# Optimization experiments

Hardware: AMD Instinct MI355X
Metric: run time of the kernel (lower is better)

## Reference

```python
import jax, jax.numpy as jnp
import numpy as np

N_NODES = 50000
N_EDGES = 800000
FEAT = 64
HID = 128
N_TYPES = 4
N_REL = 3
N_LAYERS = 2
LN_EPS = 1e-5


def setup_inputs() -> dict:
    key = jax.random.key(0)
    ks = jax.random.split(key, 20)
    inp = {
        "z": jax.random.randint(ks[0], (N_NODES,), 0, 100, dtype=jnp.int32),
        "node_type": jax.random.randint(ks[1], (N_NODES,), 0, N_TYPES, dtype=jnp.int32),
        "edge_index": jax.random.randint(ks[2], (2, N_EDGES), 0, N_NODES, dtype=jnp.int32),
        "edge_type": jax.random.randint(ks[3], (N_EDGES,), 0, N_REL, dtype=jnp.int32),
        # learned parameters
        "z_embed": jax.random.normal(ks[4], (100, FEAT), jnp.float32),
        "enc_w1": jax.random.normal(ks[5], (N_TYPES, FEAT, HID), jnp.float32) * 0.05,
        "enc_b1": jnp.zeros((N_TYPES, HID), jnp.float32),
        "enc_w2": jax.random.normal(ks[6], (N_TYPES, HID, HID), jnp.float32) * 0.05,
        "enc_b2": jnp.zeros((N_TYPES, HID), jnp.float32),
        "lin_w": jax.random.normal(ks[7], (N_LAYERS, HID, HID), jnp.float32) * 0.05,
        "lin_b": jnp.zeros((N_LAYERS, HID), jnp.float32),
        "rel_w": jax.random.normal(ks[8], (N_LAYERS, N_REL, HID, HID), jnp.float32) * 0.05,
        "ln_g": jnp.ones((N_LAYERS, HID), jnp.float32),
        "ln_b": jnp.zeros((N_LAYERS, HID), jnp.float32),
        "reg_w": jax.random.normal(ks[9], (HID, 1), jnp.float32) * 0.05,
        "reg_b": jnp.zeros((1,), jnp.float32),
    }
    return inp


def _layer_norm(x, g, b):
    mu = jnp.mean(x, axis=-1, keepdims=True)
    var = jnp.mean((x - mu) ** 2, axis=-1, keepdims=True)
    return (x - mu) * jax.lax.rsqrt(var + LN_EPS) * g + b


def reference(z, node_type, edge_index, edge_type, z_embed, enc_w1, enc_b1,
              enc_w2, enc_b2, lin_w, lin_b, rel_w, ln_g, ln_b, reg_w, reg_b):
    n = z.shape[0]
    # FeatureBuilder (site_ads=None path): atomic-number embedding lookup
    raw = z_embed[z]  # [N, FEAT]
    # TypeSpecificEncoder: run all 4 type MLPs, select per node by node_type
    h = jax.nn.relu(jnp.einsum('nd,tdh->nth', raw, enc_w1) + enc_b1)  # [N,T,H]
    enc_all = jnp.einsum('nth,tho->nto', h, enc_w2) + enc_b2           # [N,T,H]
    x = jnp.take_along_axis(enc_all, node_type[:, None, None].astype(jnp.int32), axis=1)[:, 0, :]

    src, dst = edge_index[0], edge_index[1]
    deg = jax.ops.segment_sum(jnp.ones((edge_type.shape[0],), x.dtype), dst, num_segments=n)
    deg = jnp.clip(deg, 1.0, None)[:, None]  # [N,1]

    for l in range(N_LAYERS):
        out = jnp.zeros_like(x)
        x_src = x[src]  # [E, H] gathered source features
        for r in range(N_REL):
            mask = (edge_type == r).astype(x.dtype)[:, None]
            msg = (x_src * mask) @ rel_w[l, r]  # [E, H]
            out = out + jax.ops.segment_sum(msg, dst, num_segments=n)
        out = out / deg
        x = _layer_norm(x @ lin_w[l] + lin_b[l] + out, ln_g[l], ln_b[l])

    pooled = jnp.mean(x, axis=0)  # mean pooling, mask = all ones
    return pooled @ reg_w + reg_b  # [1]
```

## Files before the change

kernel.cpp:

```cpp
#include <hip/hip_runtime.h>

#define N_NODES 50000
#define N_EDGES 800000
#define FEAT 64
#define HID 128
#define N_TYPES 4
#define N_REL 3
#define N_LAYERS 2
#define LN_EPS 1e-5f
#define NROWS 50016
#define NG32 1563
#define CAP 64
#define NBKT 196
#define CAP1 4608
#define EPB 4096
#define BINCAP 56
#define WT_STRIDE 136

typedef __attribute__((ext_vector_type(8))) short bf16x8;
typedef __attribute__((ext_vector_type(16))) float f32x16;

static __device__ inline unsigned short f2bf(float f) {
    unsigned int u = __float_as_uint(f);
    return (unsigned short)((u + 0x7fffu + ((u >> 16) & 1u)) >> 16);
}
static __device__ inline unsigned int packbf2(float lo, float hi) {
    return (unsigned int)f2bf(lo) | ((unsigned int)f2bf(hi) << 16);
}

__global__ __launch_bounds__(256) void bin1_kernel(const int* __restrict__ src,
                                                   const int* __restrict__ dst,
                                                   const int* __restrict__ et,
                                                   int* __restrict__ bcnt,
                                                   int* __restrict__ bucket) {
    __shared__ int lbin[NBKT * BINCAP];
    __shared__ int lcnt[NBKT];
    __shared__ int lbase[NBKT];
    for (int i = threadIdx.x; i < NBKT; i += 256) lcnt[i] = 0;
    __syncthreads();
    int base = blockIdx.x * EPB;
#pragma unroll
    for (int i = 0; i < EPB / 256; ++i) {
        int e = base + i * 256 + threadIdx.x;
        if (e < N_EDGES) {
            int d = dst[e];
            int b = d >> 8;
            int v = src[e] | (et[e] << 16) | ((d & 255) << 18);
            int pos = atomicAdd(&lcnt[b], 1);
            if (pos < BINCAP) lbin[b * BINCAP + pos] = v;
        }
    }
    __syncthreads();
    if (threadIdx.x < NBKT) {
        int c = min(lcnt[threadIdx.x], BINCAP);
        lcnt[threadIdx.x] = c;
        lbase[threadIdx.x] = atomicAdd(&bcnt[threadIdx.x], c);
    }
    __syncthreads();
    int wv = threadIdx.x >> 6, ln = threadIdx.x & 63;
    for (int b = wv; b < NBKT; b += 4) {
        int c = lcnt[b];
        if (ln < c) {
            int gp = lbase[b] + ln;
            if (gp < CAP1) bucket[b * CAP1 + gp] = lbin[b * BINCAP + ln];
        }
    }
}

__global__ __launch_bounds__(256) void build2_kernel(const int* __restrict__ bcnt,
                                                     const int* __restrict__ bucket,
                                                     int* __restrict__ cnt,
                                                     int* __restrict__ payload) {
    __shared__ int lcnt[256];
    lcnt[threadIdx.x] = 0;
    __syncthreads();
    int b = blockIdx.x;
    int n0 = b << 8;
    int cb = min(bcnt[b], CAP1);
    const int* bk = bucket + b * CAP1;
    for (int i = threadIdx.x; i < cb; i += 256) {
        int v = bk[i];
        int dl = (v >> 18) & 255;
        int pos = atomicAdd(&lcnt[dl], 1);
        if (pos < CAP) payload[((n0 + dl) << 6) + pos] = v & 0x3FFFF;
    }
    __syncthreads();
    int node = n0 + threadIdx.x;
    if (node < N_NODES) cnt[node] = min(lcnt[threadIdx.x], CAP);
}

__global__ __launch_bounds__(256) void prep_weights_kernel(const float* __restrict__ rel_w,
                                                           const float* __restrict__ lin_w,
                                                           unsigned short* __restrict__ wbuf) {
    int idx = blockIdx.x * 256 + threadIdx.x;
    if (idx >= 2 * 4 * HID * HID) return;
    int k = idx & 127;
    int col = (idx >> 7) & 127;
    int lm = idx >> 14;
    int l = lm >> 2, mat = lm & 3;
    float w = (mat < 3) ? rel_w[(((size_t)l * 3 + mat) * HID + k) * HID + col]
                        : lin_w[((size_t)l * HID + k) * HID + col];
    wbuf[(size_t)lm * HID * WT_STRIDE + col * WT_STRIDE + k] = f2bf(w);
}

__global__ __launch_bounds__(128) void enc_table_kernel(const float* __restrict__ z_embed,
                                                        const float* __restrict__ w1,
                                                        const float* __restrict__ b1,
                                                        const float* __restrict__ w2,
                                                        const float* __restrict__ b2,
                                                        unsigned short* __restrict__ xt) {
    int zi = blockIdx.x >> 2;
    int t = blockIdx.x & 3;
    int j = threadIdx.x;
    __shared__ float h[HID];
    float acc = b1[t * HID + j];
#pragma unroll 8
    for (int k = 0; k < FEAT; ++k)
        acc = fmaf(z_embed[zi * FEAT + k], w1[((size_t)t * FEAT + k) * HID + j], acc);
    h[j] = fmaxf(acc, 0.0f);
    __syncthreads();
    float acc2 = b2[t * HID + j];
#pragma unroll 8
    for (int k = 0; k < HID; ++k)
        acc2 = fmaf(h[k], w2[(size_t)t * HID * HID + k * HID + j], acc2);
    xt[blockIdx.x * HID + j] = f2bf(acc2);
}

__global__ __launch_bounds__(256) void node_fill_kernel(const int* __restrict__ z,
                                                        const int* __restrict__ nt,
                                                        const unsigned int* __restrict__ xtu,
                                                        unsigned int* __restrict__ xbu) {
    int idx = blockIdx.x * blockDim.x + threadIdx.x;
    int node = idx >> 6;
    if (node >= N_NODES) return;
    int lane = idx & 63;
    int combo = z[node] * 4 + nt[node];
    xbu[node * 64 + lane] = xtu[combo * 64 + lane];
}

__global__ __launch_bounds__(256) void gather3_kernel(const int* __restrict__ cnt,
                                                      const int* __restrict__ payload,
                                                      const uint4* __restrict__ xb4,
                                                      uint4* __restrict__ s0,
                                                      uint4* __restrict__ s1,
                                                      uint4* __restrict__ s2) {
    int tid = blockIdx.x * 256 + threadIdx.x;
    int node = tid >> 4;
    int l16 = tid & 15;
    int cn = min(cnt[node], CAP);
    float inv = 1.0f / (float)max(cn, 1);
    const int* pl = payload + (node << 6);
    float a0[8] = {}, a1[8] = {}, a2[8] = {};

    int e = 0;
    for (; e + 2 <= cn; e += 2) {
        int pA = pl[e];
        int pB = pl[e + 1];
        uint4 vA = xb4[(pA & 0xffff) * 16 + l16];
        uint4 vB = xb4[(pB & 0xffff) * 16 + l16];
        float fA[8] = {__uint_as_float(vA.x << 16), __uint_as_float(vA.x & 0xffff0000u),
                       __uint_as_float(vA.y << 16), __uint_as_float(vA.y & 0xffff0000u),
                       __uint_as_float(vA.z << 16), __uint_as_float(vA.z & 0xffff0000u),
                       __uint_as_float(vA.w << 16), __uint_as_float(vA.w & 0xffff0000u)};
        float fB[8] = {__uint_as_float(vB.x << 16), __uint_as_float(vB.x & 0xffff0000u),
                       __uint_as_float(vB.y << 16), __uint_as_float(vB.y & 0xffff0000u),
                       __uint_as_float(vB.z << 16), __uint_as_float(vB.z & 0xffff0000u),
                       __uint_as_float(vB.w << 16), __uint_as_float(vB.w & 0xffff0000u)};
        int rA = pA >> 16, rB = pB >> 16;
#pragma unroll
        for (int j = 0; j < 8; ++j) {
            if (rA == 0) a0[j] += fA[j];
            else if (rA == 1) a1[j] += fA[j];
            else a2[j] += fA[j];
            if (rB == 0) a0[j] += fB[j];
            else if (rB == 1) a1[j] += fB[j];
            else a2[j] += fB[j];
        }
    }
    if (e < cn) {
        int p = pl[e];
        uint4 v = xb4[(p & 0xffff) * 16 + l16];
        float f[8] = {__uint_as_float(v.x << 16), __uint_as_float(v.x & 0xffff0000u),
                      __uint_as_float(v.y << 16), __uint_as_float(v.y & 0xffff0000u),
                      __uint_as_float(v.z << 16), __uint_as_float(v.z & 0xffff0000u),
                      __uint_as_float(v.w << 16), __uint_as_float(v.w & 0xffff0000u)};
        int r = p >> 16;
#pragma unroll
        for (int j = 0; j < 8; ++j) {
            if (r == 0) a0[j] += f[j];
            else if (r == 1) a1[j] += f[j];
            else a2[j] += f[j];
        }
    }
    int o = node * 16 + l16;
    uint4 w;
    w.x = packbf2(a0[0] * inv, a0[1] * inv); w.y = packbf2(a0[2] * inv, a0[3] * inv);
    w.z = packbf2(a0[4] * inv, a0[5] * inv); w.w = packbf2(a0[6] * inv, a0[7] * inv);
    s0[o] = w;
    w.x = packbf2(a1[0] * inv, a1[1] * inv); w.y = packbf2(a1[2] * inv, a1[3] * inv);
    w.z = packbf2(a1[4] * inv, a1[5] * inv); w.w = packbf2(a1[6] * inv, a1[7] * inv);
    s1[o] = w;
    w.x = packbf2(a2[0] * inv, a2[1] * inv); w.y = packbf2(a2[2] * inv, a2[3] * inv);
    w.z = packbf2(a2[4] * inv, a2[5] * inv); w.w = packbf2(a2[6] * inv, a2[7] * inv);
    s2[o] = w;
}

__global__ __launch_bounds__(512) void fused_layer_kernel(
    const unsigned short* __restrict__ s0, const unsigned short* __restrict__ s1,
    const unsigned short* __restrict__ s2, unsigned short* __restrict__ xb,
    const uint4* __restrict__ wbuf, const float* __restrict__ lb,
    const float* __restrict__ lng, const float* __restrict__ lnb,
    float* __restrict__ pooled, int do_pool) {
    __shared__ __align__(16) unsigned short Wt[4 * HID * WT_STRIDE];
    __shared__ float csh[3 * HID];
    __shared__ float pooled_sh[HID];

    if (threadIdx.x < HID) {
        pooled_sh[threadIdx.x] = 0.0f;
        csh[threadIdx.x] = lb[threadIdx.x];
        csh[HID + threadIdx.x] = lng[threadIdx.x];
        csh[2 * HID + threadIdx.x] = lnb[threadIdx.x];
    }
    uint4* wt4 = (uint4*)Wt;
#pragma unroll
    for (int i = 0; i < 17; ++i)
        wt4[i * 512 + threadIdx.x] = wbuf[i * 512 + threadIdx.x];
    __syncthreads();

    int wave = threadIdx.x >> 6;
    int lane = threadIdx.x & 63;
    int n32 = lane & 31;
    int hf = lane >> 5;

    float pacc[4] = {0.f, 0.f, 0.f, 0.f};

    for (int g = wave * gridDim.x + blockIdx.x; g < NG32; g += gridDim.x * 8) {
        int node0 = g * 32;
        f32x16 acc[4];
#pragma unroll
        for (int ct = 0; ct < 4; ++ct)
#pragma unroll
            for (int i = 0; i < 16; ++i) acc[ct][i] = 0.0f;

#pragma unroll 1
        for (int mat = 0; mat < 4; ++mat) {
            const unsigned short* asrc = (mat == 0) ? s0 : (mat == 1) ? s1
                                       : (mat == 2) ? s2 : xb;
            const unsigned short* arow = asrc + (size_t)(node0 + n32) * HID + hf * 8;
            const unsigned short* wm = Wt + mat * (HID * WT_STRIDE) + n32 * WT_STRIDE + hf * 8;
#pragma unroll 2
            for (int t = 0; t < 8; ++t) {
                bf16x8 a = *(const bf16x8*)(arow + t * 16);
#pragma unroll
                for (int ct = 0; ct < 4; ++ct) {
                    bf16x8 b = *(const bf16x8*)(wm + ct * 32 * WT_STRIDE + t * 16);
                    acc[ct] = __builtin_amdgcn_mfma_f32_32x32x16_bf16(a, b, acc[ct], 0, 0, 0);
                }
            }
        }
#pragma unroll
        for (int reg = 0; reg < 16; ++reg) {
            int row = node0 + (reg & 3) + 8 * (reg >> 2) + 4 * hf;
            float v[4];
            float s = 0.f, q = 0.f;
#pragma unroll
            for (int ct = 0; ct < 4; ++ct) {
                v[ct] = acc[ct][reg] + csh[ct * 32 + n32];
                s += v[ct];
                q += v[ct] * v[ct];
            }
#pragma unroll
            for (int mk = 1; mk < 32; mk <<= 1) {
                s += __shfl_xor(s, mk);
                q += __shfl_xor(q, mk);
            }
            float mu = s * (1.0f / HID);
            float rstd = rsqrtf(q * (1.0f / HID) - mu * mu + LN_EPS);
#pragma unroll
            for (int ct = 0; ct < 4; ++ct) {
                int col = ct * 32 + n32;
                float outv = (v[ct] - mu) * rstd * csh[HID + col] + csh[2 * HID + col];
                if (do_pool) {
                    if (row < N_NODES) pacc[ct] += outv;
                } else {
                    xb[(size_t)row * HID + col] = f2bf(outv);
                }
            }
        }
    }

    if (do_pool) {
#pragma unroll
        for (int ct = 0; ct < 4; ++ct) {
            float t = pacc[ct] + __shfl_xor(pacc[ct], 32);
            if (hf == 0) atomicAdd(&pooled_sh[ct * 32 + n32], t);
        }
        __syncthreads();
        if (threadIdx.x < HID) atomicAdd(&pooled[threadIdx.x], pooled_sh[threadIdx.x]);
    }
}

__global__ void final_kernel(const float* __restrict__ pooled, const float* __restrict__ reg_w,
                             const float* __restrict__ reg_b, float* __restrict__ out) {
    int lane = threadIdx.x;
    float s = pooled[lane] * reg_w[lane] + pooled[64 + lane] * reg_w[64 + lane];
#pragma unroll
    for (int o = 32; o; o >>= 1) s += __shfl_down(s, o);
    if (lane == 0) out[0] = s * (1.0f / N_NODES) + reg_b[0];
}

extern "C" void kernel_launch(void* const* d_in, const int* in_sizes, int n_in,
                              void* d_out, int out_size, void* d_ws, size_t ws_size,
                              hipStream_t stream) {
    const int* z = (const int*)d_in[0];
    const int* nt = (const int*)d_in[1];
    const int* ei = (const int*)d_in[2];
    const int* et = (const int*)d_in[3];
    const float* z_embed = (const float*)d_in[4];
    const float* enc_w1 = (const float*)d_in[5];
    const float* enc_b1 = (const float*)d_in[6];
    const float* enc_w2 = (const float*)d_in[7];
    const float* enc_b2 = (const float*)d_in[8];
    const float* lin_w = (const float*)d_in[9];
    const float* lin_b = (const float*)d_in[10];
    const float* rel_w = (const float*)d_in[11];
    const float* ln_g = (const float*)d_in[12];
    const float* ln_b = (const float*)d_in[13];
    const float* reg_w = (const float*)d_in[14];
    const float* reg_b = (const float*)d_in[15];
    float* out = (float*)d_out;

    const size_t NHb = (size_t)NROWS * HID;
    char* p = (char*)d_ws;
    unsigned short* xb = (unsigned short*)p;    p += NHb * 2;
    unsigned short* s0 = (unsigned short*)p;    p += NHb * 2;
    unsigned short* s1 = (unsigned short*)p;    p += NHb * 2;
    unsigned short* s2 = (unsigned short*)p;    p += NHb * 2;
    unsigned short* wbuf = (unsigned short*)p;  p += (size_t)8 * HID * WT_STRIDE * 2;
    unsigned short* xt = (unsigned short*)p;    p += 400 * HID * 2;
    float* pooled = (float*)p;                  p += HID * 4;
    int* cnt = (int*)p;                         p += N_NODES * 4;
    int* bcnt = (int*)p;                        p += NBKT * 4;
    int* bucket = (int*)p;                      p += (size_t)NBKT * CAP1 * 4;
    int* payload = (int*)p;                     p += (size_t)N_NODES * CAP * 4;

    const int* src = ei;
    const int* dst = ei + N_EDGES;

    hipMemsetAsync(bcnt, 0, NBKT * sizeof(int), stream);
    hipMemsetAsync(pooled, 0, HID * sizeof(float), stream);
    bin1_kernel<<<NBKT, 256, 0, stream>>>(src, dst, et, bcnt, bucket);
    build2_kernel<<<NBKT, 256, 0, stream>>>(bcnt, bucket, cnt, payload);

    prep_weights_kernel<<<512, 256, 0, stream>>>(rel_w, lin_w, wbuf);
    enc_table_kernel<<<400, 128, 0, stream>>>(z_embed, enc_w1, enc_b1, enc_w2, enc_b2, xt);
    node_fill_kernel<<<(N_NODES * 64 + 255) / 256, 256, 0, stream>>>(
        z, nt, (const unsigned int*)xt, (unsigned int*)xb);

    for (int l = 0; l < N_LAYERS; ++l) {
        gather3_kernel<<<3125, 256, 0, stream>>>(cnt, payload, (const uint4*)xb,
                                                 (uint4*)s0, (uint4*)s1, (uint4*)s2);
        const uint4* wl = (const uint4*)(wbuf + (size_t)l * 4 * HID * WT_STRIDE);
        fused_layer_kernel<<<256, 512, 0, stream>>>(
            s0, s1, s2, xb, wl, lin_b + l * HID,
            ln_g + l * HID, ln_b + l * HID, pooled, l == N_LAYERS - 1 ? 1 : 0);
    }

    final_kernel<<<1, 64, 0, stream>>>(pooled, reg_w, reg_b, out);
}
```

Measured before the change: 275.8 us.

## Precompute layer-1 messages per node combo and fuse gather with layernorm

Node features before layer 1 depend only on the (z, node_type) pair, which has 400 possible values. The change therefore precomputes each combo's relation-transformed rows and linear projection in small tables. Layer 1 becomes a gather of table rows plus an inline layernorm, replacing the node fill, the three-way scatter buffers and the fused matmul layer. Combo ids are packed into the edge payload during the CSR build. This removes a full layer of tensor-core GEMMs and intermediate traffic, at the cost of an extra combo kernel and a small scalar table kernel.

```diff
diff --git a/kernel.cpp b/kernel.cpp
--- a/kernel.cpp
+++ b/kernel.cpp
@@ -15,6 +15,7 @@
 #define CAP1 4608
 #define EPB 4096
 #define BINCAP 56
+#define NCOMBO 400
 #define WT_STRIDE 136
 
 typedef __attribute__((ext_vector_type(8))) short bf16x8;
@@ -26,6 +27,13 @@
 }
 static __device__ inline unsigned int packbf2(float lo, float hi) {
     return (unsigned int)f2bf(lo) | ((unsigned int)f2bf(hi) << 16);
+}
+
+__global__ __launch_bounds__(256) void combo_kernel(const int* __restrict__ z,
+                                                    const int* __restrict__ nt,
+                                                    unsigned short* __restrict__ combo) {
+    int i = blockIdx.x * 256 + threadIdx.x;
+    if (i < N_NODES) combo[i] = (unsigned short)(z[i] * 4 + nt[i]);
 }
 
 __global__ __launch_bounds__(256) void bin1_kernel(const int* __restrict__ src,
@@ -69,6 +77,7 @@
 
 __global__ __launch_bounds__(256) void build2_kernel(const int* __restrict__ bcnt,
                                                      const int* __restrict__ bucket,
+                                                     const unsigned short* __restrict__ combo,
                                                      int* __restrict__ cnt,
                                                      int* __restrict__ payload) {
     __shared__ int lcnt[256];
@@ -81,26 +90,14 @@
     for (int i = threadIdx.x; i < cb; i += 256) {
         int v = bk[i];
         int dl = (v >> 18) & 255;
+        int sc = v & 0xffff;
         int pos = atomicAdd(&lcnt[dl], 1);
-        if (pos < CAP) payload[((n0 + dl) << 6) + pos] = v & 0x3FFFF;
+        if (pos < CAP)
+            payload[((n0 + dl) << 6) + pos] = (v & 0x3FFFF) | ((int)combo[sc] << 18);
     }
     __syncthreads();
     int node = n0 + threadIdx.x;
     if (node < N_NODES) cnt[node] = min(lcnt[threadIdx.x], CAP);
-}
-
-__global__ __launch_bounds__(256) void prep_weights_kernel(const float* __restrict__ rel_w,
-                                                           const float* __restrict__ lin_w,
-                                                           unsigned short* __restrict__ wbuf) {
-    int idx = blockIdx.x * 256 + threadIdx.x;
-    if (idx >= 2 * 4 * HID * HID) return;
-    int k = idx & 127;
-    int col = (idx >> 7) & 127;
-    int lm = idx >> 14;
-    int l = lm >> 2, mat = lm & 3;
-    float w = (mat < 3) ? rel_w[(((size_t)l * 3 + mat) * HID + k) * HID + col]
-                        : lin_w[((size_t)l * HID + k) * HID + col];
-    wbuf[(size_t)lm * HID * WT_STRIDE + col * WT_STRIDE + k] = f2bf(w);
 }
 
 __global__ __launch_bounds__(128) void enc_table_kernel(const float* __restrict__ z_embed,
@@ -126,16 +123,106 @@
     xt[blockIdx.x * HID + j] = f2bf(acc2);
 }
 
-__global__ __launch_bounds__(256) void node_fill_kernel(const int* __restrict__ z,
-                                                        const int* __restrict__ nt,
-                                                        const unsigned int* __restrict__ xtu,
-                                                        unsigned int* __restrict__ xbu) {
-    int idx = blockIdx.x * blockDim.x + threadIdx.x;
-    int node = idx >> 6;
-    if (node >= N_NODES) return;
-    int lane = idx & 63;
-    int combo = z[node] * 4 + nt[node];
-    xbu[node * 64 + lane] = xtu[combo * 64 + lane];
+__global__ __launch_bounds__(128) void rel_table_kernel(const unsigned short* __restrict__ xt,
+                                                        const float* __restrict__ rel_w,
+                                                        const float* __restrict__ lin_w,
+                                                        const float* __restrict__ lin_b,
+                                                        unsigned short* __restrict__ ytab,
+                                                        float* __restrict__ lintab) {
+    int c = blockIdx.x;
+    int j = threadIdx.x;
+    __shared__ float xrow[HID];
+    xrow[j] = __uint_as_float((unsigned int)xt[c * HID + j] << 16);
+    __syncthreads();
+#pragma unroll 1
+    for (int r = 0; r < N_REL; ++r) {
+        float acc = 0.f;
+        const float* W = rel_w + (size_t)r * HID * HID;
+#pragma unroll 8
+        for (int k = 0; k < HID; ++k) acc = fmaf(xrow[k], W[k * HID + j], acc);
+        ytab[(size_t)(r * NCOMBO + c) * HID + j] = f2bf(acc);
+    }
+    float acc = lin_b[j];
+#pragma unroll 8
+    for (int k = 0; k < HID; ++k) acc = fmaf(xrow[k], lin_w[k * HID + j], acc);
+    lintab[c * HID + j] = acc;
+}
+
+__global__ __launch_bounds__(256) void prep_weights_kernel(const float* __restrict__ rel_w,
+                                                           const float* __restrict__ lin_w,
+                                                           unsigned short* __restrict__ wbuf) {
+    int idx = blockIdx.x * 256 + threadIdx.x;
+    if (idx >= 2 * 4 * HID * HID) return;
+    int k = idx & 127;
+    int col = (idx >> 7) & 127;
+    int lm = idx >> 14;
+    int l = lm >> 2, mat = lm & 3;
+    float w = (mat < 3) ? rel_w[(((size_t)l * 3 + mat) * HID + k) * HID + col]
+                        : lin_w[((size_t)l * HID + k) * HID + col];
+    wbuf[(size_t)lm * HID * WT_STRIDE + col * WT_STRIDE + k] = f2bf(w);
+}
+
+__global__ __launch_bounds__(256) void gather_ln1_kernel(
+    const int* __restrict__ cnt, const int* __restrict__ payload,
+    const uint4* __restrict__ ytab4, const float* __restrict__ lintab,
+    const unsigned short* __restrict__ combo, const float* __restrict__ lng,
+    const float* __restrict__ lnb, uint4* __restrict__ xb4) {
+    int tid = blockIdx.x * 256 + threadIdx.x;
+    int node = tid >> 4;
+    int l16 = tid & 15;
+    int cn = cnt[node];
+    float inv = 1.0f / (float)max(cn, 1);
+    const int* pl = payload + (node << 6);
+    float a[8] = {};
+    int e = 0;
+    for (; e + 2 <= cn; e += 2) {
+        int pA = pl[e], pB = pl[e + 1];
+        uint4 vA = ytab4[((((pA >> 16) & 3) * NCOMBO + (pA >> 18)) << 4) + l16];
+        uint4 vB = ytab4[((((pB >> 16) & 3) * NCOMBO + (pB >> 18)) << 4) + l16];
+        a[0] += __uint_as_float(vA.x << 16) + __uint_as_float(vB.x << 16);
+        a[1] += __uint_as_float(vA.x & 0xffff0000u) + __uint_as_float(vB.x & 0xffff0000u);
+        a[2] += __uint_as_float(vA.y << 16) + __uint_as_float(vB.y << 16);
+        a[3] += __uint_as_float(vA.y & 0xffff0000u) + __uint_as_float(vB.y & 0xffff0000u);
+        a[4] += __uint_as_float(vA.z << 16) + __uint_as_float(vB.z << 16);
+        a[5] += __uint_as_float(vA.z & 0xffff0000u) + __uint_as_float(vB.z & 0xffff0000u);
+        a[6] += __uint_as_float(vA.w << 16) + __uint_as_float(vB.w << 16);
+        a[7] += __uint_as_float(vA.w & 0xffff0000u) + __uint_as_float(vB.w & 0xffff0000u);
+    }
+    if (e < cn) {
+        int p = pl[e];
+        uint4 v = ytab4[((((p >> 16) & 3) * NCOMBO + (p >> 18)) << 4) + l16];
+        a[0] += __uint_as_float(v.x << 16);
+        a[1] += __uint_as_float(v.x & 0xffff0000u);
+        a[2] += __uint_as_float(v.y << 16);
+        a[3] += __uint_as_float(v.y & 0xffff0000u);
+        a[4] += __uint_as_float(v.z << 16);
+        a[5] += __uint_as_float(v.z & 0xffff0000u);
+        a[6] += __uint_as_float(v.w << 16);
+        a[7] += __uint_as_float(v.w & 0xffff0000u);
+    }
+    const float* lrow = lintab + (int)combo[node] * HID + l16 * 8;
+    float v[8], s = 0.f, q = 0.f;
+#pragma unroll
+    for (int j = 0; j < 8; ++j) {
+        v[j] = fmaf(a[j], inv, lrow[j]);
+        s += v[j];
+        q += v[j] * v[j];
+    }
+#pragma unroll
+    for (int mk = 1; mk < 16; mk <<= 1) {
+        s += __shfl_xor(s, mk);
+        q += __shfl_xor(q, mk);
+    }
+    float mu = s * (1.0f / HID);
+    float rstd = rsqrtf(q * (1.0f / HID) - mu * mu + LN_EPS);
+    const float* g8 = lng + l16 * 8;
+    const float* b8 = lnb + l16 * 8;
+    uint4 w;
+    w.x = packbf2((v[0] - mu) * rstd * g8[0] + b8[0], (v[1] - mu) * rstd * g8[1] + b8[1]);
+    w.y = packbf2((v[2] - mu) * rstd * g8[2] + b8[2], (v[3] - mu) * rstd * g8[3] + b8[3]);
+    w.z = packbf2((v[4] - mu) * rstd * g8[4] + b8[4], (v[5] - mu) * rstd * g8[5] + b8[5]);
+    w.w = packbf2((v[6] - mu) * rstd * g8[6] + b8[6], (v[7] - mu) * rstd * g8[7] + b8[7]);
+    xb4[(node << 4) + l16] = w;
 }
 
 __global__ __launch_bounds__(256) void gather3_kernel(const int* __restrict__ cnt,
@@ -147,7 +234,7 @@
     int tid = blockIdx.x * 256 + threadIdx.x;
     int node = tid >> 4;
     int l16 = tid & 15;
-    int cn = min(cnt[node], CAP);
+    int cn = cnt[node];
     float inv = 1.0f / (float)max(cn, 1);
     const int* pl = payload + (node << 6);
     float a0[8] = {}, a1[8] = {}, a2[8] = {};
@@ -166,7 +253,7 @@
                        __uint_as_float(vB.y << 16), __uint_as_float(vB.y & 0xffff0000u),
                        __uint_as_float(vB.z << 16), __uint_as_float(vB.z & 0xffff0000u),
                        __uint_as_float(vB.w << 16), __uint_as_float(vB.w & 0xffff0000u)};
-        int rA = pA >> 16, rB = pB >> 16;
+        int rA = (pA >> 16) & 3, rB = (pB >> 16) & 3;
 #pragma unroll
         for (int j = 0; j < 8; ++j) {
             if (rA == 0) a0[j] += fA[j];
@@ -184,7 +271,7 @@
                       __uint_as_float(v.y << 16), __uint_as_float(v.y & 0xffff0000u),
                       __uint_as_float(v.z << 16), __uint_as_float(v.z & 0xffff0000u),
                       __uint_as_float(v.w << 16), __uint_as_float(v.w & 0xffff0000u)};
-        int r = p >> 16;
+        int r = (p >> 16) & 3;
 #pragma unroll
         for (int j = 0; j < 8; ++j) {
             if (r == 0) a0[j] += f[j];
@@ -337,7 +424,10 @@
     unsigned short* s1 = (unsigned short*)p;    p += NHb * 2;
     unsigned short* s2 = (unsigned short*)p;    p += NHb * 2;
     unsigned short* wbuf = (unsigned short*)p;  p += (size_t)8 * HID * WT_STRIDE * 2;
-    unsigned short* xt = (unsigned short*)p;    p += 400 * HID * 2;
+    unsigned short* xt = (unsigned short*)p;    p += NCOMBO * HID * 2;
+    unsigned short* ytab = (unsigned short*)p;  p += (size_t)N_REL * NCOMBO * HID * 2;
+    float* lintab = (float*)p;                  p += NCOMBO * HID * 4;
+    unsigned short* combo = (unsigned short*)p; p += N_NODES * 2;
     float* pooled = (float*)p;                  p += HID * 4;
     int* cnt = (int*)p;                         p += N_NODES * 4;
     int* bcnt = (int*)p;                        p += NBKT * 4;
@@ -349,22 +439,21 @@
 
     hipMemsetAsync(bcnt, 0, NBKT * sizeof(int), stream);
     hipMemsetAsync(pooled, 0, HID * sizeof(float), stream);
+    combo_kernel<<<NBKT, 256, 0, stream>>>(z, nt, combo);
     bin1_kernel<<<NBKT, 256, 0, stream>>>(src, dst, et, bcnt, bucket);
-    build2_kernel<<<NBKT, 256, 0, stream>>>(bcnt, bucket, cnt, payload);
-
+    build2_kernel<<<NBKT, 256, 0, stream>>>(bcnt, bucket, combo, cnt, payload);
+
+    enc_table_kernel<<<NCOMBO, 128, 0, stream>>>(z_embed, enc_w1, enc_b1, enc_w2, enc_b2, xt);
+    rel_table_kernel<<<NCOMBO, 128, 0, stream>>>(xt, rel_w, lin_w, lin_b, ytab, lintab);
     prep_weights_kernel<<<512, 256, 0, stream>>>(rel_w, lin_w, wbuf);
-    enc_table_kernel<<<400, 128, 0, stream>>>(z_embed, enc_w1, enc_b1, enc_w2, enc_b2, xt);
-    node_fill_kernel<<<(N_NODES * 64 + 255) / 256, 256, 0, stream>>>(
-        z, nt, (const unsigned int*)xt, (unsigned int*)xb);
-
-    for (int l = 0; l < N_LAYERS; ++l) {
-        gather3_kernel<<<3125, 256, 0, stream>>>(cnt, payload, (const uint4*)xb,
-                                                 (uint4*)s0, (uint4*)s1, (uint4*)s2);
-        const uint4* wl = (const uint4*)(wbuf + (size_t)l * 4 * HID * WT_STRIDE);
-        fused_layer_kernel<<<256, 512, 0, stream>>>(
-            s0, s1, s2, xb, wl, lin_b + l * HID,
-            ln_g + l * HID, ln_b + l * HID, pooled, l == N_LAYERS - 1 ? 1 : 0);
-    }
+
+    gather_ln1_kernel<<<3125, 256, 0, stream>>>(cnt, payload, (const uint4*)ytab, lintab,
+                                                combo, ln_g, ln_b, (uint4*)xb);
+    gather3_kernel<<<3125, 256, 0, stream>>>(cnt, payload, (const uint4*)xb,
+                                             (uint4*)s0, (uint4*)s1, (uint4*)s2);
+    const uint4* wl = (const uint4*)(wbuf + (size_t)1 * 4 * HID * WT_STRIDE);
+    fused_layer_kernel<<<256, 512, 0, stream>>>(
+        s0, s1, s2, xb, wl, lin_b + HID, ln_g + HID, ln_b + HID, pooled, 1);
 
     final_kernel<<<1, 64, 0, stream>>>(pooled, reg_w, reg_b, out);
 }
```

Result: faster. 254.1 us (-7.9%).
